# Optimization experiments

Measured on AMD Instinct MI355X. Metric: run time of the kernel, lower is better.

The kernel has to match this reference:

```python
import jax, jax.numpy as jnp
import numpy as np

HEADS = 4
HEAD_DIM = 128  # GATConv out_channels
NEG_SLOPE_ATT = 0.2   # GATConv internal leaky relu
NEG_SLOPE_ACT = 0.01  # nn.LeakyReLU() default


def gat_conv(x, edge_index, W, att_src, att_dst, bias):
    # x: [N, F]; edge_index: [2, E] (row 0 = src j, row 1 = dst i)
    N = x.shape[0]
    h = (x @ W).reshape(N, HEADS, HEAD_DIM)            # [N, H, C]
    loops = jnp.arange(N, dtype=edge_index.dtype)
    src = jnp.concatenate([edge_index[0], loops])      # add self loops
    dst = jnp.concatenate([edge_index[1], loops])
    a_src = jnp.einsum('nhc,hc->nh', h, att_src)       # [N, H]
    a_dst = jnp.einsum('nhc,hc->nh', h, att_dst)
    e = jax.nn.leaky_relu(a_src[src] + a_dst[dst], NEG_SLOPE_ATT)  # [E', H]
    # segment softmax over incoming edges of each dst node
    emax = jax.ops.segment_max(e, dst, num_segments=N)
    ex = jnp.exp(e - emax[dst])
    denom = jax.ops.segment_sum(ex, dst, num_segments=N)
    alpha = ex / (denom[dst] + 1e-16)                  # [E', H]
    msg = h[src] * alpha[:, :, None]                   # [E', H, C]
    out = jax.ops.segment_sum(msg, dst, num_segments=N)
    return out.reshape(N, HEADS * HEAD_DIM) + bias     # [N, H*C]


def branch(x, edge_index, W, att_src, att_dst, bias, fc1_w, fc1_b):
    h = gat_conv(x, edge_index, W, att_src, att_dst, bias)
    h = jax.nn.leaky_relu(h, NEG_SLOPE_ACT)
    g = jnp.mean(h, axis=0, keepdims=True)             # global mean pool, batch all zeros -> [1, H*C]
    g = jax.nn.leaky_relu(g @ fc1_w + fc1_b, NEG_SLOPE_ACT)
    return g  # dropout is identity in eval mode


def setup_inputs() -> dict:
    key = jax.random.key(0)
    ks = jax.random.split(key, 10)
    N, E, F = 20000, 320000, 512
    HC = HEADS * HEAD_DIM
    s = 1.0 / np.sqrt(F)
    return {
        'x': jax.random.normal(ks[0], (N, F), jnp.float32),
        'adj': jax.random.randint(ks[1], (2, E), 0, N, jnp.int64),
        'wt_x': jax.random.normal(ks[2], (N, F), jnp.float32),
        'wt_adj': jax.random.randint(ks[3], (2, E), 0, N, jnp.int64),
        'W': jax.random.normal(ks[4], (F, HC), jnp.float32) * s,
        'att_src': jax.random.normal(ks[5], (HEADS, HEAD_DIM), jnp.float32) * s,
        'att_dst': jax.random.normal(ks[6], (HEADS, HEAD_DIM), jnp.float32) * s,
        'bias': jnp.zeros((HC,), jnp.float32),
        'fc1_w': jax.random.normal(ks[7], (HC, 512), jnp.float32) * (1.0 / np.sqrt(HC)),
        'fc1_b': jnp.zeros((512,), jnp.float32),
    }


def reference(x, adj, wt_x, wt_adj, W, att_src, att_dst, bias, fc1_w, fc1_b):
    g = branch(x, adj, W, att_src, att_dst, bias, fc1_w, fc1_b)
    wt_g = branch(wt_x, wt_adj, W, att_src, att_dst, bias, fc1_w, fc1_b)
    xd = g - wt_g
    return jnp.concatenate([g, wt_g, xd], axis=1)  # [1, 3*512]
```

## Files before the change

kernel.cpp:

```cpp
#include <hip/hip_runtime.h>
#include <hip/hip_bf16.h>

typedef unsigned short u16;
typedef short bf16x8 __attribute__((ext_vector_type(8)));
typedef float f32x4 __attribute__((ext_vector_type(4)));
typedef float f32x2 __attribute__((ext_vector_type(2)));

__device__ __forceinline__ u16 f2b(float f) {
    unsigned x = __float_as_uint(f);
    return (u16)((x + 0x7fffu + ((x >> 16) & 1u)) >> 16);
}

__device__ __forceinline__ int pkbf(float lo, float hi) {
    return __builtin_amdgcn_perm(__float_as_uint(hi), __float_as_uint(lo), 0x07060302);
}

__global__ void cast_wt_kernel(const float* __restrict__ W, u16* __restrict__ Wt) {
    int idx = blockIdx.x * blockDim.x + threadIdx.x;
    int n = idx >> 9, k = idx & 511;
    Wt[idx] = f2b(W[k * 512 + n]);
}

__global__ __launch_bounds__(256, 2) void gemm_fused2(
    const float* __restrict__ xA, const float* __restrict__ xW, const u16* __restrict__ Bt,
    unsigned char* __restrict__ h8, const float* __restrict__ att_src,
    const float* __restrict__ att_dst, float* __restrict__ asrc, float* __restrict__ adst,
    int N, int Mpad) {
    __shared__ float lA[128 * 32];
    __shared__ u16 lB[128 * 32];
    __shared__ float sred[2][128][2];
    const int tid = threadIdx.x;
    const int w = tid >> 6, l = tid & 63;
    const int row0 = blockIdx.y * 128;
    const int head = blockIdx.x;
    const int col0 = head * 128;
    const int wr = w >> 1, wc = w & 1;
    const int mlane = l & 15, quad = l >> 4;
    const int R2v = 2 * Mpad;

    const float* src = (row0 >= Mpad) ? xW : xA;
    const int rbase = row0 - (row0 >= Mpad ? Mpad : 0);
    const int arow = (w << 3) + (l >> 3);
    const int acol = (l & 7) << 2;
    const int srow = (w << 4) + (l >> 2);
    const int scol = (l & 3) << 3;

    f32x4 acc[4][4];
#pragma unroll
    for (int i = 0; i < 4; i++)
#pragma unroll
        for (int j = 0; j < 4; j++) acc[i][j] = f32x4{0.f, 0.f, 0.f, 0.f};

    for (int k0 = 0; k0 < 512; k0 += 32) {
#pragma unroll
        for (int g = 0; g < 4; ++g) {
            int lrow = rbase + g * 32 + arow;
            lrow = min(lrow, N - 1);
            const float* ga = src + (size_t)lrow * 512 + k0 + acol;
            float* la = lA + (g * 32 + (w << 3)) * 32;
            __builtin_amdgcn_global_load_lds((const __attribute__((address_space(1))) void*)ga,
                                             (__attribute__((address_space(3))) void*)la, 16, 0, 0);
        }
#pragma unroll
        for (int s = 0; s < 2; ++s) {
            const u16* gb = Bt + (size_t)(col0 + s * 64 + srow) * 512 + (k0 + scol);
            u16* lb = lB + s * 2048 + w * 512;
            __builtin_amdgcn_global_load_lds((const __attribute__((address_space(1))) void*)gb,
                                             (__attribute__((address_space(3))) void*)lb, 16, 0, 0);
        }
        __syncthreads();
        bf16x8 af[4], bfr[4];
#pragma unroll
        for (int i = 0; i < 4; i++) {
            const float* ap = &lA[(wr * 64 + i * 16 + mlane) * 32 + quad * 8];
            float4 f0 = *(const float4*)ap;
            float4 f1 = *(const float4*)(ap + 4);
            int* ai = (int*)&af[i];
            ai[0] = pkbf(f0.x, f0.y);
            ai[1] = pkbf(f0.z, f0.w);
            ai[2] = pkbf(f1.x, f1.y);
            ai[3] = pkbf(f1.z, f1.w);
            bfr[i] = *(const bf16x8*)&lB[(wc * 64 + i * 16 + mlane) * 32 + quad * 8];
        }
#pragma unroll
        for (int i = 0; i < 4; i++)
#pragma unroll
            for (int j = 0; j < 4; j++)
                acc[i][j] = __builtin_amdgcn_mfma_f32_16x16x32_bf16(af[i], bfr[j], acc[i][j], 0, 0, 0);
        __syncthreads();
    }

    float as_j[4], ad_j[4];
#pragma unroll
    for (int j = 0; j < 4; j++) {
        as_j[j] = att_src[col0 + wc * 64 + j * 16 + mlane];
        ad_j[j] = att_dst[col0 + wc * 64 + j * 16 + mlane];
    }
#pragma unroll
    for (int i = 0; i < 4; i++) {
#pragma unroll
        for (int r = 0; r < 4; r++) {
            float vs = 0.f, vd = 0.f;
#pragma unroll
            for (int j = 0; j < 4; j++) {
                float hv = acc[i][j][r];
                vs += hv * as_j[j];
                vd += hv * ad_j[j];
            }
#pragma unroll
            for (int o = 8; o >= 1; o >>= 1) {
                vs += __shfl_xor(vs, o);
                vd += __shfl_xor(vd, o);
            }
            if (mlane == 0) {
                int lrow = wr * 64 + i * 16 + quad * 4 + r;
                sred[0][lrow][wc] = vs;
                sred[1][lrow][wc] = vd;
            }
        }
    }
#pragma unroll
    for (int i = 0; i < 4; i++)
#pragma unroll
        for (int j = 0; j < 4; j++)
#pragma unroll
            for (int r = 0; r < 4; r++) {
                int rg = row0 + wr * 64 + i * 16 + quad * 4 + r;
                int cc = wc * 64 + j * 16 + mlane;
                float v = acc[i][j][r];
                unsigned pk = __builtin_amdgcn_cvt_pk_fp8_f32(v, v, 0, false);
                h8[(((size_t)(head * R2v + rg)) << 7) + cc] = (unsigned char)(pk & 0xff);
            }
    __syncthreads();
    {
        int row = tid & 127, which = tid >> 7;
        int rg = row0 + row;
        float v = sred[which][row][0] + sred[which][row][1];
        (which ? adst : asrc)[head * R2v + rg] = v;
    }
}

__global__ void csr_count(const int* __restrict__ adj, const int* __restrict__ wadj,
                          int E, int Mpad, int* __restrict__ deg) {
    int i = blockIdx.x * blockDim.x + threadIdx.x;
    if (i < 2 * E) {
        int d = (i < E) ? adj[E + i] : (wadj[E + (i - E)] + Mpad);
        atomicAdd(&deg[d], 1);
    }
}

__global__ __launch_bounds__(256) void scanA(const int* __restrict__ deg, int* __restrict__ off,
                                             int* __restrict__ bsum, int n, int N, int Mpad) {
    __shared__ int wsum[4];
    int tid = threadIdx.x, lane = tid & 63, wid = tid >> 6;
    int i = blockIdx.x * 256 + tid;
    int valid = (i < N) || (i >= Mpad && i < Mpad + N);
    int d = (i < n) ? deg[i] + (valid ? 1 : 0) : 0;
    int x = d;
#pragma unroll
    for (int o = 1; o < 64; o <<= 1) {
        int y = __shfl_up(x, (unsigned)o, 64);
        if (lane >= o) x += y;
    }
    if (lane == 63) wsum[wid] = x;
    __syncthreads();
    int woff = 0;
    for (int j = 0; j < wid; ++j) woff += wsum[j];
    if (i < n) off[i] = woff + x - d;
    if (tid == 255) bsum[blockIdx.x] = woff + x;
}

__global__ __launch_bounds__(256) void scanB(const int* __restrict__ bsum, int* __restrict__ bbase,
                                             int nb, int* __restrict__ off, int n) {
    __shared__ int wsum[4];
    int tid = threadIdx.x, lane = tid & 63, wid = tid >> 6;
    int d = (tid < nb) ? bsum[tid] : 0;
    int x = d;
#pragma unroll
    for (int o = 1; o < 64; o <<= 1) {
        int y = __shfl_up(x, (unsigned)o, 64);
        if (lane >= o) x += y;
    }
    if (lane == 63) wsum[wid] = x;
    __syncthreads();
    int woff = 0;
    for (int j = 0; j < wid; ++j) woff += wsum[j];
    int excl = woff + x - d;
    if (tid < nb) bbase[tid] = excl;
    if (tid == nb - 1) off[n] = excl + d;
}

__global__ void scanC(int* __restrict__ off, const int* __restrict__ bbase,
                      int* __restrict__ cursor, int* __restrict__ csrc, int n, int N, int Mpad) {
    int i = blockIdx.x * blockDim.x + threadIdx.x;
    if (i < n) {
        int o = off[i] + bbase[i >> 8];
        off[i] = o;
        int valid = (i < N) || (i >= Mpad && i < Mpad + N);
        if (valid) csrc[o] = i;
        cursor[i] = o + valid;
    }
}

__global__ void csr_scatter(const int* __restrict__ adj, const int* __restrict__ wadj,
                            int E, int Mpad, int* __restrict__ cursor, int* __restrict__ csrc) {
    int i = blockIdx.x * blockDim.x + threadIdx.x;
    if (i < 2 * E) {
        int s, d;
        if (i < E) {
            s = adj[i];
            d = adj[E + i];
        } else {
            s = wadj[i - E] + Mpad;
            d = wadj[E + (i - E)] + Mpad;
        }
        int p = atomicAdd(&cursor[d], 1);
        csrc[p] = s;
    }
}

__device__ __forceinline__ void edgeH(int hr, bool valid, float ad,
                                      const float* __restrict__ ash,
                                      const unsigned char* __restrict__ h8h, int ch,
                                      float* acc, float& dsum) {
    float e = ash[hr] + ad;
    e = fmaxf(e, 0.2f * e);
    float ex = __expf(e);
    ex = valid ? ex : 0.f;
    dsum += ex;
    int2 hv = *(const int2*)(h8h + (((size_t)hr) << 7) + ch);
    f32x2 f01 = __builtin_amdgcn_cvt_pk_f32_fp8(hv.x, false);
    f32x2 f23 = __builtin_amdgcn_cvt_pk_f32_fp8(hv.x, true);
    f32x2 f45 = __builtin_amdgcn_cvt_pk_f32_fp8(hv.y, false);
    f32x2 f67 = __builtin_amdgcn_cvt_pk_f32_fp8(hv.y, true);
    acc[0] += ex * f01.x; acc[1] += ex * f01.y;
    acc[2] += ex * f23.x; acc[3] += ex * f23.y;
    acc[4] += ex * f45.x; acc[5] += ex * f45.y;
    acc[6] += ex * f67.x; acc[7] += ex * f67.y;
}

__global__ __launch_bounds__(256) void gat_aggregate7(
    const unsigned char* __restrict__ h8, const float* __restrict__ asrc,
    const float* __restrict__ adst, const int* __restrict__ off, const int* __restrict__ csrc,
    const float* __restrict__ bias, float* __restrict__ partAB, int Mpad) {
    const int R2 = 2 * Mpad;
    __shared__ float spool[256];
    int tid = threadIdx.x;
    spool[tid] = 0.f;
    __syncthreads();
    int wv = tid >> 6, l = tid & 63;
    int g = l >> 4;
    int ch = (l & 15) << 3;
    int head = (blockIdx.x & 7) >> 1;
    const unsigned char* h8h = h8 + (((size_t)head * R2) << 7);
    const float* ash = asrc + (size_t)head * R2;
    const float* adh = adst + (size_t)head * R2;
    float bb[8];
#pragma unroll
    for (int k = 0; k < 8; ++k) bb[k] = bias[head * 128 + ch + k];
    float poolA[8] = {0.f, 0.f, 0.f, 0.f, 0.f, 0.f, 0.f, 0.f};
    float poolB[8] = {0.f, 0.f, 0.f, 0.f, 0.f, 0.f, 0.f, 0.f};

    int widx = ((((blockIdx.x >> 3) << 1) | (blockIdx.x & 1)) << 2) + wv;
    const int nquad = R2 >> 2;
    for (int q = widx; q < nquad; q += gridDim.x) {
        int d0 = q << 2;
        int dg = d0 + g;
        int qa = off[dg], qb = off[dg + 1];
        int n = qb - qa;
        float ad = adh[dg];
        float acc[8] = {0.f, 0.f, 0.f, 0.f, 0.f, 0.f, 0.f, 0.f};
        float dsum = 0.f;
        int nmax = n;
        nmax = max(nmax, __shfl_xor(nmax, 16));
        nmax = max(nmax, __shfl_xor(nmax, 32));
        int i = 0;
        for (; i + 2 <= nmax; i += 2) {
            bool v0 = i < n, v1 = i + 1 < n;
            int i0 = v0 ? qa + i : 0;
            int i1 = v1 ? qa + i + 1 : 0;
            int h0 = csrc[i0];
            int h1 = csrc[i1];
            edgeH(h0, v0, ad, ash, h8h, ch, acc, dsum);
            edgeH(h1, v1, ad, ash, h8h, ch, acc, dsum);
        }
        if (i < nmax) {
            bool v0 = i < n;
            int i0 = v0 ? qa + i : 0;
            edgeH(csrc[i0], v0, ad, ash, h8h, ch, acc, dsum);
        }
        if (n > 0) {
            float inv = 1.f / (dsum + 1e-16f);
            if (d0 >= Mpad) {
#pragma unroll
                for (int k = 0; k < 8; ++k) {
                    float o = acc[k] * inv + bb[k];
                    poolB[k] += fmaxf(o, 0.01f * o);
                }
            } else {
#pragma unroll
                for (int k = 0; k < 8; ++k) {
                    float o = acc[k] * inv + bb[k];
                    poolA[k] += fmaxf(o, 0.01f * o);
                }
            }
        }
    }
#pragma unroll
    for (int k = 0; k < 8; ++k) {
        atomicAdd(&spool[ch + k], poolA[k]);
        atomicAdd(&spool[128 + ch + k], poolB[k]);
    }
    __syncthreads();
    {
        int base = (blockIdx.x & 63) << 9;
        int c = tid & 127;
        float v = spool[tid];
        float* dp = (tid < 128) ? (partAB + base + head * 128 + c)
                                : (partAB + 64 * 512 + base + head * 128 + c);
        atomicAdd(dp, v);
    }
}

__global__ __launch_bounds__(256) void fc_final2(
    const float* __restrict__ partAB, const float* __restrict__ w, const float* __restrict__ b,
    float* __restrict__ out, float invN) {
    __shared__ float gA[512], gB[512];
    __shared__ float rA[256], rB[256];
    int t = threadIdx.x;
    for (int i = t; i < 512; i += 256) {
        float sA = 0.f, sB = 0.f;
        for (int r = 0; r < 64; ++r) {
            sA += partAB[r * 512 + i];
            sB += partAB[64 * 512 + r * 512 + i];
        }
        gA[i] = sA * invN;
        gB[i] = sB * invN;
    }
    __syncthreads();
    int jj = t & 31, ks = t >> 5;
    int j = blockIdx.x * 32 + jj;
    float sA = 0.f, sB = 0.f;
    for (int k = ks * 64; k < ks * 64 + 64; ++k) {
        float wv = w[k * 512 + j];
        sA += gA[k] * wv;
        sB += gB[k] * wv;
    }
    rA[t] = sA;
    rB[t] = sB;
    __syncthreads();
    if (ks == 0) {
#pragma unroll
        for (int s2 = 1; s2 < 8; ++s2) {
            sA += rA[jj + 32 * s2];
            sB += rB[jj + 32 * s2];
        }
        sA += b[j];
        sB += b[j];
        sA = sA >= 0.f ? sA : 0.01f * sA;
        sB = sB >= 0.f ? sB : 0.01f * sB;
        out[j] = sA;
        out[512 + j] = sB;
        out[1024 + j] = sA - sB;
    }
}

extern "C" void kernel_launch(void* const* d_in, const int* in_sizes, int n_in,
                              void* d_out, int out_size, void* d_ws, size_t ws_size,
                              hipStream_t stream) {
    const float* x = (const float*)d_in[0];
    const int* adj = (const int*)d_in[1];
    const float* wtx = (const float*)d_in[2];
    const int* wadj = (const int*)d_in[3];
    const float* W = (const float*)d_in[4];
    const float* att_s = (const float*)d_in[5];
    const float* att_d = (const float*)d_in[6];
    const float* bias = (const float*)d_in[7];
    const float* fc1w = (const float*)d_in[8];
    const float* fc1b = (const float*)d_in[9];
    float* out = (float*)d_out;

    const int N = in_sizes[0] / 512;
    const int E = in_sizes[1] / 2;
    const int Mpad = ((N + 127) / 128) * 128;
    const int R2 = 2 * Mpad;
    const int nb = (R2 + 255) / 256;

    char* p = (char*)d_ws;
    auto alloc = [&](size_t bytes) -> char* {
        char* r = p;
        p += (bytes + 255) & ~(size_t)255;
        return r;
    };
    unsigned char* h8 = (unsigned char*)alloc((size_t)R2 * 512);
    u16* Wt = (u16*)alloc(512 * 512 * 2);
    float* asrc = (float*)alloc((size_t)R2 * 4 * 4);
    float* adst = (float*)alloc((size_t)R2 * 4 * 4);
    int* deg = (int*)alloc((size_t)R2 * 4);
    int* off = (int*)alloc((size_t)(R2 + 1) * 4);
    int* cursor = (int*)alloc((size_t)R2 * 4);
    int* bsum = (int*)alloc(256 * 4);
    int* bbase = (int*)alloc(256 * 4);
    int* csrc = (int*)alloc((size_t)2 * (E + N) * 4);
    float* partAB = (float*)alloc((size_t)2 * 64 * 512 * 4);

    hipMemsetAsync(partAB, 0, (size_t)2 * 64 * 512 * 4, stream);
    hipMemsetAsync(deg, 0, (size_t)R2 * 4, stream);
    cast_wt_kernel<<<(512 * 512) / 256, 256, 0, stream>>>(W, Wt);

    csr_count<<<(2 * E + 255) / 256, 256, 0, stream>>>(adj, wadj, E, Mpad, deg);
    scanA<<<nb, 256, 0, stream>>>(deg, off, bsum, R2, N, Mpad);
    scanB<<<1, 256, 0, stream>>>(bsum, bbase, nb, off, R2);
    scanC<<<nb, 256, 0, stream>>>(off, bbase, cursor, csrc, R2, N, Mpad);
    csr_scatter<<<(2 * E + 255) / 256, 256, 0, stream>>>(adj, wadj, E, Mpad, cursor, csrc);

    dim3 gg(4, R2 / 128, 1);
    gemm_fused2<<<gg, 256, 0, stream>>>(x, wtx, Wt, h8, att_s, att_d, asrc, adst, N, Mpad);

    gat_aggregate7<<<2048, 256, 0, stream>>>(h8, asrc, adst, off, csrc, bias, partAB, Mpad);

    fc_final2<<<16, 256, 0, stream>>>(partAB, fc1w, fc1b, out, 1.0f / (float)N);
}
```

Before: 372.1 us.

## Assign one destination node per wavefront, splitting its edges across lane groups

The aggregation kernel now gives each wavefront a single destination node and spreads that node's incoming edges across the four 16-lane groups, eight edges per iteration. The old mapping gave each group its own node and padded every group to the wavefront's maximum degree. Partial accumulators and softmax denominators are combined with cross-lane shuffles, and only the first group adds to the shared pool. This targets divergence from uneven degrees and keeps more gathers in flight. It adds shuffle reductions per node and leaves lanes idle when a node has fewer than eight edges.

```diff
diff --git a/kernel.cpp b/kernel.cpp
--- a/kernel.cpp
+++ b/kernel.cpp
@@ -239,7 +239,7 @@
     acc[6] += ex * f67.x; acc[7] += ex * f67.y;
 }
 
-__global__ __launch_bounds__(256) void gat_aggregate7(
+__global__ __launch_bounds__(256) void gat_aggregate8(
     const unsigned char* __restrict__ h8, const float* __restrict__ asrc,
     const float* __restrict__ adst, const int* __restrict__ off, const int* __restrict__ csrc,
     const float* __restrict__ bias, float* __restrict__ partAB, int Mpad) {
@@ -262,36 +262,31 @@
     float poolB[8] = {0.f, 0.f, 0.f, 0.f, 0.f, 0.f, 0.f, 0.f};
 
     int widx = ((((blockIdx.x >> 3) << 1) | (blockIdx.x & 1)) << 2) + wv;
-    const int nquad = R2 >> 2;
-    for (int q = widx; q < nquad; q += gridDim.x) {
-        int d0 = q << 2;
-        int dg = d0 + g;
-        int qa = off[dg], qb = off[dg + 1];
-        int n = qb - qa;
-        float ad = adh[dg];
+    const int stride = gridDim.x;
+    for (int d = widx; d < R2; d += stride) {
+        int qa = off[d];
+        int n = off[d + 1] - qa;
+        float ad = adh[d];
         float acc[8] = {0.f, 0.f, 0.f, 0.f, 0.f, 0.f, 0.f, 0.f};
         float dsum = 0.f;
-        int nmax = n;
-        nmax = max(nmax, __shfl_xor(nmax, 16));
-        nmax = max(nmax, __shfl_xor(nmax, 32));
-        int i = 0;
-        for (; i + 2 <= nmax; i += 2) {
-            bool v0 = i < n, v1 = i + 1 < n;
-            int i0 = v0 ? qa + i : 0;
-            int i1 = v1 ? qa + i + 1 : 0;
-            int h0 = csrc[i0];
-            int h1 = csrc[i1];
-            edgeH(h0, v0, ad, ash, h8h, ch, acc, dsum);
-            edgeH(h1, v1, ad, ash, h8h, ch, acc, dsum);
-        }
-        if (i < nmax) {
-            bool v0 = i < n;
-            int i0 = v0 ? qa + i : 0;
-            edgeH(csrc[i0], v0, ad, ash, h8h, ch, acc, dsum);
+        for (int base = 0; base < n; base += 8) {
+            int i0 = base + (g << 1);
+            bool v0 = i0 < n, v1 = i0 + 1 < n;
+            int e0 = csrc[qa + (v0 ? i0 : 0)];
+            int e1 = csrc[qa + (v1 ? i0 + 1 : 0)];
+            edgeH(e0, v0, ad, ash, h8h, ch, acc, dsum);
+            edgeH(e1, v1, ad, ash, h8h, ch, acc, dsum);
+        }
+        dsum += __shfl_xor(dsum, 16);
+        dsum += __shfl_xor(dsum, 32);
+#pragma unroll
+        for (int k = 0; k < 8; ++k) {
+            acc[k] += __shfl_xor(acc[k], 16);
+            acc[k] += __shfl_xor(acc[k], 32);
         }
         if (n > 0) {
             float inv = 1.f / (dsum + 1e-16f);
-            if (d0 >= Mpad) {
+            if (d >= Mpad) {
 #pragma unroll
                 for (int k = 0; k < 8; ++k) {
                     float o = acc[k] * inv + bb[k];
@@ -306,10 +301,12 @@
             }
         }
     }
-#pragma unroll
-    for (int k = 0; k < 8; ++k) {
-        atomicAdd(&spool[ch + k], poolA[k]);
-        atomicAdd(&spool[128 + ch + k], poolB[k]);
+    if (l < 16) {
+#pragma unroll
+        for (int k = 0; k < 8; ++k) {
+            atomicAdd(&spool[ch + k], poolA[k]);
+            atomicAdd(&spool[128 + ch + k], poolB[k]);
+        }
     }
     __syncthreads();
     {
@@ -417,7 +414,7 @@
     dim3 gg(4, R2 / 128, 1);
     gemm_fused2<<<gg, 256, 0, stream>>>(x, wtx, Wt, h8, att_s, att_d, asrc, adst, N, Mpad);
 
-    gat_aggregate7<<<2048, 256, 0, stream>>>(h8, asrc, adst, off, csrc, bias, partAB, Mpad);
+    gat_aggregate8<<<2048, 256, 0, stream>>>(h8, asrc, adst, off, csrc, bias, partAB, Mpad);
 
     fc_final2<<<16, 256, 0, stream>>>(partAB, fc1w, fc1b, out, 1.0f / (float)N);
 }
```

After: 366.4 us. Within noise of the previous version (-1.5%).
